# Kernel tuning notes

Measured on AMD Instinct MI355X. Metric: run time of the kernel, lower is better.

## Reference

```python
import jax, jax.numpy as jnp
import numpy as np

N_NODES = 100000
N_EDGES = 1000000
IN_DIM = 32
HID_DIM = 64
NUM_REL = 2
NUM_CLASSES = 2


def setup_inputs() -> dict:
    key = jax.random.key(0)
    ks = jax.random.split(key, 12)
    x = jax.random.normal(ks[0], (N_NODES, IN_DIM), dtype=jnp.float32)
    edge_index = jax.random.randint(ks[1], (2, N_EDGES), 0, N_NODES, dtype=jnp.int32)
    edge_attr = jax.random.randint(ks[2], (N_EDGES, 2), 0, NUM_REL, dtype=jnp.int32)
    s1 = 1.0 / np.sqrt(IN_DIM)
    s2 = 1.0 / np.sqrt(HID_DIM)
    W1 = jax.random.normal(ks[3], (NUM_REL, IN_DIM, HID_DIM), dtype=jnp.float32) * s1
    root1 = jax.random.normal(ks[4], (IN_DIM, HID_DIM), dtype=jnp.float32) * s1
    b1 = jnp.zeros((HID_DIM,), dtype=jnp.float32)
    W2 = jax.random.normal(ks[5], (NUM_REL, HID_DIM, HID_DIM), dtype=jnp.float32) * s2
    root2 = jax.random.normal(ks[6], (HID_DIM, HID_DIM), dtype=jnp.float32) * s2
    b2 = jnp.zeros((HID_DIM,), dtype=jnp.float32)
    Wc = jax.random.normal(ks[7], (HID_DIM, NUM_CLASSES), dtype=jnp.float32) * s2
    bc = jnp.zeros((NUM_CLASSES,), dtype=jnp.float32)
    return {"x": x, "edge_index": edge_index, "edge_attr": edge_attr,
            "W1": W1, "root1": root1, "b1": b1,
            "W2": W2, "root2": root2, "b2": b2,
            "Wc": Wc, "bc": bc}


def _rgcn_conv(x, src, dst, edge_type, W, root, b):
    # PyG RGCNConv (aggr='mean'): out = x @ root + b + sum_r mean_agg_r(x_j) @ W_r
    n = x.shape[0]
    xs = x[src]  # [E, F] gather, shared across relations
    out = x @ root + b
    for r in range(W.shape[0]):
        m = (edge_type == r).astype(x.dtype)  # [E]
        s = jax.ops.segment_sum(xs * m[:, None], dst, num_segments=n)  # [N, F]
        cnt = jax.ops.segment_sum(m, dst, num_segments=n)  # [N]
        h = s / jnp.maximum(cnt, 1.0)[:, None]
        out = out + h @ W[r]
    return out


def reference(x, edge_index, edge_attr, W1, root1, b1, W2, root2, b2, Wc, bc):
    edge_type = edge_attr[:, -1].astype(jnp.int32)
    src, dst = edge_index[0], edge_index[1]
    h = jax.nn.relu(_rgcn_conv(x, src, dst, edge_type, W1, root1, b1))
    # dropout(p=0.2) is identity in eval mode
    h = jax.nn.relu(_rgcn_conv(h, src, dst, edge_type, W2, root2, b2))
    return h @ Wc + bc
```

## Files before the change

kernel.cpp:

```cpp
#include <hip/hip_runtime.h>

#define N_NODES 100000
#define N_EDGES 1000000
#define IN_DIM 32
#define HID_DIM 64
#define N2 (2 * N_NODES)
#define NRANGE 8
#define RNODES (N_NODES / NRANGE)
#define ECHUNK 2048


__global__ __launch_bounds__(256) void k_count(
    const int* __restrict__ ei, const int* __restrict__ ea,
    int* __restrict__ deg)
{
    int range = blockIdx.x & (NRANGE - 1);
    int chunk = blockIdx.x >> 3;
    int lo = range * RNODES;
    int e0 = chunk * ECHUNK;
    int e1 = min(e0 + ECHUNK, N_EDGES);
    for (int e = e0 + threadIdx.x; e < e1; e += 256) {
        int dst = ei[N_EDGES + e];
        if ((unsigned)(dst - lo) < (unsigned)RNODES) {
            int rel = ea[2 * e + 1];
            atomicAdd(&deg[rel * N_NODES + dst], 1);
        }
    }
}

__global__ __launch_bounds__(256) void k_scan_local(
    const int* __restrict__ deg, int* __restrict__ offs, int* __restrict__ bsum)
{
    int t = threadIdx.x;
    int i = blockIdx.x * 256 + t;
    int v = (i < N2) ? deg[i] : 0;
    int lane = t & 63, w = t >> 6;
    int s = v;
#pragma unroll
    for (int off = 1; off < 64; off <<= 1) {
        int u = __shfl_up(s, off);
        if (lane >= off) s += u;
    }
    __shared__ int wsum[4];
    if (lane == 63) wsum[w] = s;
    __syncthreads();
    int add = 0;
    for (int ww = 0; ww < w; ++ww) add += wsum[ww];
    s += add;
    if (i < N2) offs[i] = s - v;
    if (t == 255) bsum[blockIdx.x] = s;
}

__global__ __launch_bounds__(64) void k_scan_blocks(int* __restrict__ bsum, int nblk)
{
    int lane = threadIdx.x;
    int carry = 0;
    for (int base = 0; base < nblk; base += 64) {
        int i = base + lane;
        int v = (i < nblk) ? bsum[i] : 0;
        int s = v;
#pragma unroll
        for (int off = 1; off < 64; off <<= 1) {
            int u = __shfl_up(s, off);
            if (lane >= off) s += u;
        }
        if (i < nblk) bsum[i] = carry + s - v;
        carry += __shfl(s, 63);
    }
}

__global__ __launch_bounds__(256) void k_scan_add(
    const int* __restrict__ offs, const int* __restrict__ bsum,
    const int* __restrict__ deg,
    int* __restrict__ cursor, int2* __restrict__ od)
{
    int i = blockIdx.x * 256 + threadIdx.x;
    if (i >= N2) return;
    int o = offs[i] + bsum[i >> 8];
    cursor[i] = o;
    od[i] = make_int2(o, deg[i]);
}

__global__ __launch_bounds__(256) void k_fill(
    const int* __restrict__ ei, const int* __restrict__ ea,
    int* __restrict__ cursor, int* __restrict__ elist)
{
    int range = blockIdx.x & (NRANGE - 1);
    int chunk = blockIdx.x >> 3;
    int lo = range * RNODES;
    int e0 = chunk * ECHUNK;
    int e1 = min(e0 + ECHUNK, N_EDGES);
    for (int e = e0 + threadIdx.x; e < e1; e += 256) {
        int dst = ei[N_EDGES + e];
        if ((unsigned)(dst - lo) < (unsigned)RNODES) {
            int rel = ea[2 * e + 1];
            int src = ei[e];
            int pos = atomicAdd(&cursor[rel * N_NODES + dst], 1);
            elist[pos] = src;
        }
    }
}


__device__ __forceinline__ unsigned short f2bf(float f) {
    unsigned u = __float_as_uint(f);
    return (unsigned short)((u + 0x7FFFu + ((u >> 16) & 1u)) >> 16);
}

#define ACC4(acc, v, wa, wb, wc_, wd) \
    acc = fmaf((v).x, wa, acc);       \
    acc = fmaf((v).y, wb, acc);       \
    acc = fmaf((v).z, wc_, acc);      \
    acc = fmaf((v).w, wd, acc);

#define MACC4(A, v, m)                \
    A.x = fmaf((v).x, m, A.x);        \
    A.y = fmaf((v).y, m, A.y);        \
    A.z = fmaf((v).z, m, A.z);        \
    A.w = fmaf((v).w, m, A.w);

#define BUNPACK(v_, u) {                           \
    v_.x = __uint_as_float((u).x << 16);           \
    v_.y = __uint_as_float((u).x & 0xFFFF0000u);   \
    v_.z = __uint_as_float((u).y << 16);           \
    v_.w = __uint_as_float((u).y & 0xFFFF0000u);   \
}

#define BMACC4(A, u, m) { float4 v_; BUNPACK(v_, u) MACC4(A, v_, m) }


__global__ __launch_bounds__(512, 4) void k_gemm1(
    const float* __restrict__ x,
    const float* __restrict__ root1,
    const float* __restrict__ W1,
    const float* __restrict__ b1,
    float* __restrict__ R,
    unsigned short* __restrict__ Y)
{
    __shared__ float wR[IN_DIM * HID_DIM];
    __shared__ float w0[IN_DIM * HID_DIM];
    __shared__ float w1s[IN_DIM * HID_DIM];
    int tid = threadIdx.x;
    for (int i = tid; i < IN_DIM * HID_DIM; i += 512) {
        wR[i]  = root1[i];
        w0[i]  = W1[i];
        w1s[i] = W1[IN_DIM * HID_DIM + i];
    }
    __syncthreads();

    int j  = tid & 63;
    int n0 = __builtin_amdgcn_readfirstlane(blockIdx.x * 32 + ((tid >> 6) << 2));
    const float* px = x + (size_t)n0 * IN_DIM;

    float accR0 = 0, accR1 = 0, accR2 = 0, accR3 = 0;
    float acc00 = 0, acc01 = 0, acc02 = 0, acc03 = 0;
    float acc10 = 0, acc11 = 0, acc12 = 0, acc13 = 0;

#pragma unroll 1
    for (int kk = 0; kk < IN_DIM / 4; ++kk) {
        int kbase = kk * 4;
        float4 xv0 = *(const float4*)(px + 0 * IN_DIM + kbase);
        float4 xv1 = *(const float4*)(px + 1 * IN_DIM + kbase);
        float4 xv2 = *(const float4*)(px + 2 * IN_DIM + kbase);
        float4 xv3 = *(const float4*)(px + 3 * IN_DIM + kbase);
        int wb_i = kbase * 64 + j;
        float wRa = wR[wb_i], wRb = wR[wb_i + 64], wRc = wR[wb_i + 128], wRd = wR[wb_i + 192];
        float w0a = w0[wb_i], w0b = w0[wb_i + 64], w0c = w0[wb_i + 128], w0d = w0[wb_i + 192];
        float w1a = w1s[wb_i], w1b = w1s[wb_i + 64], w1c = w1s[wb_i + 128], w1d = w1s[wb_i + 192];

        ACC4(accR0, xv0, wRa, wRb, wRc, wRd)
        ACC4(accR1, xv1, wRa, wRb, wRc, wRd)
        ACC4(accR2, xv2, wRa, wRb, wRc, wRd)
        ACC4(accR3, xv3, wRa, wRb, wRc, wRd)
        ACC4(acc00, xv0, w0a, w0b, w0c, w0d)
        ACC4(acc01, xv1, w0a, w0b, w0c, w0d)
        ACC4(acc02, xv2, w0a, w0b, w0c, w0d)
        ACC4(acc03, xv3, w0a, w0b, w0c, w0d)
        ACC4(acc10, xv0, w1a, w1b, w1c, w1d)
        ACC4(acc11, xv1, w1a, w1b, w1c, w1d)
        ACC4(acc12, xv2, w1a, w1b, w1c, w1d)
        ACC4(acc13, xv3, w1a, w1b, w1c, w1d)
    }

    float bj = b1[j];
    R[(size_t)(n0 + 0) * HID_DIM + j] = accR0 + bj;
    R[(size_t)(n0 + 1) * HID_DIM + j] = accR1 + bj;
    R[(size_t)(n0 + 2) * HID_DIM + j] = accR2 + bj;
    R[(size_t)(n0 + 3) * HID_DIM + j] = accR3 + bj;
    unsigned short* Y0 = Y;
    unsigned short* Y1 = Y + (size_t)N_NODES * HID_DIM;
    Y0[(size_t)(n0 + 0) * HID_DIM + j] = f2bf(acc00);
    Y0[(size_t)(n0 + 1) * HID_DIM + j] = f2bf(acc01);
    Y0[(size_t)(n0 + 2) * HID_DIM + j] = f2bf(acc02);
    Y0[(size_t)(n0 + 3) * HID_DIM + j] = f2bf(acc03);
    Y1[(size_t)(n0 + 0) * HID_DIM + j] = f2bf(acc10);
    Y1[(size_t)(n0 + 1) * HID_DIM + j] = f2bf(acc11);
    Y1[(size_t)(n0 + 2) * HID_DIM + j] = f2bf(acc12);
    Y1[(size_t)(n0 + 3) * HID_DIM + j] = f2bf(acc13);
}

__global__ __launch_bounds__(512, 4) void k_gemm2(
    const unsigned short* __restrict__ h1b,
    const float* __restrict__ root2,
    const float* __restrict__ W2,
    const float* __restrict__ b2,
    float* __restrict__ R,
    unsigned short* __restrict__ Y)
{
    __shared__ float wR[HID_DIM * HID_DIM];
    __shared__ float w0[HID_DIM * HID_DIM];
    __shared__ float w1s[HID_DIM * HID_DIM];
    int tid = threadIdx.x;
    for (int i = tid; i < HID_DIM * HID_DIM; i += 512) {
        wR[i]  = root2[i];
        w0[i]  = W2[i];
        w1s[i] = W2[HID_DIM * HID_DIM + i];
    }
    __syncthreads();

    int j  = tid & 63;
    int n0 = __builtin_amdgcn_readfirstlane(blockIdx.x * 32 + ((tid >> 6) << 2));
    const unsigned short* pb = h1b + (size_t)n0 * HID_DIM;

    float accR0 = 0, accR1 = 0, accR2 = 0, accR3 = 0;
    float acc00 = 0, acc01 = 0, acc02 = 0, acc03 = 0;
    float acc10 = 0, acc11 = 0, acc12 = 0, acc13 = 0;

#pragma unroll 1
    for (int kk = 0; kk < HID_DIM / 4; ++kk) {
        int kbase = kk * 4;
        uint2 u0 = *(const uint2*)(pb + 0 * HID_DIM + kbase);
        uint2 u1 = *(const uint2*)(pb + 1 * HID_DIM + kbase);
        uint2 u2 = *(const uint2*)(pb + 2 * HID_DIM + kbase);
        uint2 u3 = *(const uint2*)(pb + 3 * HID_DIM + kbase);
        float4 xv0, xv1, xv2, xv3;
        BUNPACK(xv0, u0) BUNPACK(xv1, u1) BUNPACK(xv2, u2) BUNPACK(xv3, u3)
        int wb_i = kbase * 64 + j;
        float wRa = wR[wb_i], wRb = wR[wb_i + 64], wRc = wR[wb_i + 128], wRd = wR[wb_i + 192];
        float w0a = w0[wb_i], w0b = w0[wb_i + 64], w0c = w0[wb_i + 128], w0d = w0[wb_i + 192];
        float w1a = w1s[wb_i], w1b = w1s[wb_i + 64], w1c = w1s[wb_i + 128], w1d = w1s[wb_i + 192];

        ACC4(accR0, xv0, wRa, wRb, wRc, wRd)
        ACC4(accR1, xv1, wRa, wRb, wRc, wRd)
        ACC4(accR2, xv2, wRa, wRb, wRc, wRd)
        ACC4(accR3, xv3, wRa, wRb, wRc, wRd)
        ACC4(acc00, xv0, w0a, w0b, w0c, w0d)
        ACC4(acc01, xv1, w0a, w0b, w0c, w0d)
        ACC4(acc02, xv2, w0a, w0b, w0c, w0d)
        ACC4(acc03, xv3, w0a, w0b, w0c, w0d)
        ACC4(acc10, xv0, w1a, w1b, w1c, w1d)
        ACC4(acc11, xv1, w1a, w1b, w1c, w1d)
        ACC4(acc12, xv2, w1a, w1b, w1c, w1d)
        ACC4(acc13, xv3, w1a, w1b, w1c, w1d)
    }

    float bj = b2[j];
    R[(size_t)(n0 + 0) * HID_DIM + j] = accR0 + bj;
    R[(size_t)(n0 + 1) * HID_DIM + j] = accR1 + bj;
    R[(size_t)(n0 + 2) * HID_DIM + j] = accR2 + bj;
    R[(size_t)(n0 + 3) * HID_DIM + j] = accR3 + bj;
    unsigned short* Y0 = Y;
    unsigned short* Y1 = Y + (size_t)N_NODES * HID_DIM;
    Y0[(size_t)(n0 + 0) * HID_DIM + j] = f2bf(acc00);
    Y0[(size_t)(n0 + 1) * HID_DIM + j] = f2bf(acc01);
    Y0[(size_t)(n0 + 2) * HID_DIM + j] = f2bf(acc02);
    Y0[(size_t)(n0 + 3) * HID_DIM + j] = f2bf(acc03);
    Y1[(size_t)(n0 + 0) * HID_DIM + j] = f2bf(acc10);
    Y1[(size_t)(n0 + 1) * HID_DIM + j] = f2bf(acc11);
    Y1[(size_t)(n0 + 2) * HID_DIM + j] = f2bf(acc12);
    Y1[(size_t)(n0 + 3) * HID_DIM + j] = f2bf(acc13);
}


__global__ __launch_bounds__(512, 8) void k_gather1(
    const unsigned short* __restrict__ Y,
    const float* __restrict__ R,
    const int2* __restrict__ od,
    const int* __restrict__ elist,
    unsigned short* __restrict__ h1b)
{
    int tid = threadIdx.x;
    int lane = tid & 63;
    int wv   = __builtin_amdgcn_readfirstlane(tid >> 6);
    int n0   = __builtin_amdgcn_readfirstlane(blockIdx.x * 32 + wv * 4);

    int sub  = lane >> 4;
    int node = n0 + sub;
    int q    = lane & 15;
    int base = lane & 48;

    const unsigned short* Y0 = Y;
    const unsigned short* Y1 = Y + (size_t)N_NODES * HID_DIM;

    int2 o0 = od[node];
    int2 o1 = od[N_NODES + node];
    int d0 = o0.y, d1 = o1.y;
    int er0 = (q < d0) ? elist[o0.x + q] : 0;
    int er1 = (q < d1) ? elist[o1.x + q] : 0;

    int dm = max(d0, d1);
    dm = max(dm, __shfl_xor(dm, 16));
    dm = max(dm, __shfl_xor(dm, 32));
    int kend = min(dm, 16);

    float4 A0 = make_float4(0.f, 0.f, 0.f, 0.f);
    float4 A1 = make_float4(0.f, 0.f, 0.f, 0.f);
    for (int k = 0; k < kend; ++k) {
        int i0 = __shfl(er0, base + k);
        int i1 = __shfl(er1, base + k);
        uint2 u0 = *(const uint2*)(Y0 + (size_t)i0 * HID_DIM + q * 4);
        uint2 u1 = *(const uint2*)(Y1 + (size_t)i1 * HID_DIM + q * 4);
        float m0 = (k < d0) ? 1.0f : 0.0f;
        float m1 = (k < d1) ? 1.0f : 0.0f;
        BMACC4(A0, u0, m0)
        BMACC4(A1, u1, m1)
    }
    if (dm > 16) {
        for (int k = 16; k < dm; ++k) {
            int i0 = 0, i1 = 0;
            if (k < d0) i0 = elist[o0.x + k];
            if (k < d1) i1 = elist[o1.x + k];
            uint2 u0 = *(const uint2*)(Y0 + (size_t)i0 * HID_DIM + q * 4);
            uint2 u1 = *(const uint2*)(Y1 + (size_t)i1 * HID_DIM + q * 4);
            float m0 = (k < d0) ? 1.0f : 0.0f;
            float m1 = (k < d1) ? 1.0f : 0.0f;
            BMACC4(A0, u0, m0)
            BMACC4(A1, u1, m1)
        }
    }
    float i0v = 1.0f / fmaxf((float)d0, 1.0f);
    float i1v = 1.0f / fmaxf((float)d1, 1.0f);
    float4 Rq = *(const float4*)(R + (size_t)node * HID_DIM + q * 4);
    ushort4 o;
    o.x = f2bf(fmaxf(Rq.x + A0.x * i0v + A1.x * i1v, 0.0f));
    o.y = f2bf(fmaxf(Rq.y + A0.y * i0v + A1.y * i1v, 0.0f));
    o.z = f2bf(fmaxf(Rq.z + A0.z * i0v + A1.z * i1v, 0.0f));
    o.w = f2bf(fmaxf(Rq.w + A0.w * i0v + A1.w * i1v, 0.0f));
    *(ushort4*)(h1b + (size_t)node * HID_DIM + q * 4) = o;
}

__global__ __launch_bounds__(512, 8) void k_gather2(
    const unsigned short* __restrict__ Y,
    const float* __restrict__ R,
    const int2* __restrict__ od,
    const int* __restrict__ elist,
    const float* __restrict__ Wc,
    const float* __restrict__ bc,
    float* __restrict__ out)
{
    int tid = threadIdx.x;
    int lane = tid & 63;
    int wv   = __builtin_amdgcn_readfirstlane(tid >> 6);
    int n0   = __builtin_amdgcn_readfirstlane(blockIdx.x * 32 + wv * 4);

    int sub  = lane >> 4;
    int node = n0 + sub;
    int q    = lane & 15;
    int base = lane & 48;

    const unsigned short* Y0 = Y;
    const unsigned short* Y1 = Y + (size_t)N_NODES * HID_DIM;

    int2 o0 = od[node];
    int2 o1 = od[N_NODES + node];
    int d0 = o0.y, d1 = o1.y;
    int er0 = (q < d0) ? elist[o0.x + q] : 0;
    int er1 = (q < d1) ? elist[o1.x + q] : 0;

    int dm = max(d0, d1);
    dm = max(dm, __shfl_xor(dm, 16));
    dm = max(dm, __shfl_xor(dm, 32));
    int kend = min(dm, 16);

    float4 A0 = make_float4(0.f, 0.f, 0.f, 0.f);
    float4 A1 = make_float4(0.f, 0.f, 0.f, 0.f);
    for (int k = 0; k < kend; ++k) {
        int i0 = __shfl(er0, base + k);
        int i1 = __shfl(er1, base + k);
        uint2 u0 = *(const uint2*)(Y0 + (size_t)i0 * HID_DIM + q * 4);
        uint2 u1 = *(const uint2*)(Y1 + (size_t)i1 * HID_DIM + q * 4);
        float m0 = (k < d0) ? 1.0f : 0.0f;
        float m1 = (k < d1) ? 1.0f : 0.0f;
        BMACC4(A0, u0, m0)
        BMACC4(A1, u1, m1)
    }
    if (dm > 16) {
        for (int k = 16; k < dm; ++k) {
            int i0 = 0, i1 = 0;
            if (k < d0) i0 = elist[o0.x + k];
            if (k < d1) i1 = elist[o1.x + k];
            uint2 u0 = *(const uint2*)(Y0 + (size_t)i0 * HID_DIM + q * 4);
            uint2 u1 = *(const uint2*)(Y1 + (size_t)i1 * HID_DIM + q * 4);
            float m0 = (k < d0) ? 1.0f : 0.0f;
            float m1 = (k < d1) ? 1.0f : 0.0f;
            BMACC4(A0, u0, m0)
            BMACC4(A1, u1, m1)
        }
    }
    float i0v = 1.0f / fmaxf((float)d0, 1.0f);
    float i1v = 1.0f / fmaxf((float)d1, 1.0f);
    float4 Rq = *(const float4*)(R + (size_t)node * HID_DIM + q * 4);
    float4 h2;
    h2.x = fmaxf(Rq.x + A0.x * i0v + A1.x * i1v, 0.0f);
    h2.y = fmaxf(Rq.y + A0.y * i0v + A1.y * i1v, 0.0f);
    h2.z = fmaxf(Rq.z + A0.z * i0v + A1.z * i1v, 0.0f);
    h2.w = fmaxf(Rq.w + A0.w * i0v + A1.w * i1v, 0.0f);

    float4 wcA = *(const float4*)(Wc + 8 * q);
    float4 wcB = *(const float4*)(Wc + 8 * q + 4);
    float v0 = h2.x * wcA.x + h2.y * wcA.z + h2.z * wcB.x + h2.w * wcB.z;
    float v1 = h2.x * wcA.y + h2.y * wcA.w + h2.z * wcB.y + h2.w * wcB.w;
#pragma unroll
    for (int off = 1; off <= 8; off <<= 1) {
        v0 += __shfl_xor(v0, off);
        v1 += __shfl_xor(v1, off);
    }
    if (q == 0) {
        out[(size_t)node * 2 + 0] = v0 + bc[0];
        out[(size_t)node * 2 + 1] = v1 + bc[1];
    }
}


extern "C" void kernel_launch(void* const* d_in, const int* in_sizes, int n_in,
                              void* d_out, int out_size, void* d_ws, size_t ws_size,
                              hipStream_t stream) {
    const float* x     = (const float*)d_in[0];
    const int*   ei    = (const int*)d_in[1];
    const int*   ea    = (const int*)d_in[2];
    const float* W1    = (const float*)d_in[3];
    const float* root1 = (const float*)d_in[4];
    const float* b1    = (const float*)d_in[5];
    const float* W2    = (const float*)d_in[6];
    const float* root2 = (const float*)d_in[7];
    const float* b2    = (const float*)d_in[8];
    const float* Wc    = (const float*)d_in[9];
    const float* bc    = (const float*)d_in[10];
    float* out = (float*)d_out;

    char* ws = (char*)d_ws;
    int*   deg    = (int*)(ws);
    int*   offs   = (int*)(ws + 800000);
    int2*  od     = (int2*)(ws + 1600000);
    int*   elist  = (int*)(ws + 3200000);
    int*   cursor = (int*)(ws + 7200000);
    int*   bsum   = (int*)(ws + 8000000);
    unsigned short* Y   = (unsigned short*)(ws + 8004096);
    float* R            = (float*)(ws + 33604096);
    unsigned short* h1b = (unsigned short*)(ws + 59204096);

    const int nblk_scan = (N2 + 255) / 256;
    const int grid_cf   = ((N_EDGES + ECHUNK - 1) / ECHUNK) * NRANGE;
    const int grid_n    = N_NODES / 32;

    hipMemsetAsync(deg, 0, (size_t)N2 * 4, stream);
    k_count<<<grid_cf, 256, 0, stream>>>(ei, ea, deg);
    k_scan_local<<<nblk_scan, 256, 0, stream>>>(deg, offs, bsum);
    k_scan_blocks<<<1, 64, 0, stream>>>(bsum, nblk_scan);
    k_scan_add<<<nblk_scan, 256, 0, stream>>>(offs, bsum, deg, cursor, od);
    k_fill<<<grid_cf, 256, 0, stream>>>(ei, ea, cursor, elist);

    k_gemm1<<<grid_n, 512, 0, stream>>>(x, root1, W1, b1, R, Y);
    k_gather1<<<grid_n, 512, 0, stream>>>(Y, R, od, elist, h1b);

    k_gemm2<<<grid_n, 512, 0, stream>>>(h1b, root2, W2, b2, R, Y);
    k_gather2<<<grid_n, 512, 0, stream>>>(Y, R, od, elist, Wc, bc, out);
}
```

Baseline: 230.9 us.

## Pack dst and relation into one word; make GEMM kernels persistent

Adds a pre-pass that packs each edge's destination and relation type into a single int, so the count and fill passes (each launched 8 times over the edge list, once per node range) read one coalesced int instead of the dst row plus a strided edge_attr column. The two per-node GEMM kernels become grid-stride persistent kernels over a fixed 768-block grid, so the weight matrices are staged into LDS fewer times. The cost is an extra kernel launch and a 4 MB write, and fewer resident blocks may hide latency less well.

```diff
diff --git a/kernel.cpp b/kernel.cpp
--- a/kernel.cpp
+++ b/kernel.cpp
@@ -8,11 +8,22 @@
 #define NRANGE 8
 #define RNODES (N_NODES / NRANGE)
 #define ECHUNK 2048
+#define NTILES (N_NODES / 32)
+#define GEMM_GRID 768
+
+
+__global__ __launch_bounds__(256) void k_rd(
+    const int* __restrict__ ei, const int* __restrict__ ea,
+    int* __restrict__ rd)
+{
+    int e = blockIdx.x * 256 + threadIdx.x;
+    if (e >= N_EDGES) return;
+    rd[e] = (ei[N_EDGES + e] << 1) | ea[2 * e + 1];
+}
 
 
 __global__ __launch_bounds__(256) void k_count(
-    const int* __restrict__ ei, const int* __restrict__ ea,
-    int* __restrict__ deg)
+    const int* __restrict__ rd, int* __restrict__ deg)
 {
     int range = blockIdx.x & (NRANGE - 1);
     int chunk = blockIdx.x >> 3;
@@ -20,11 +31,10 @@
     int e0 = chunk * ECHUNK;
     int e1 = min(e0 + ECHUNK, N_EDGES);
     for (int e = e0 + threadIdx.x; e < e1; e += 256) {
-        int dst = ei[N_EDGES + e];
-        if ((unsigned)(dst - lo) < (unsigned)RNODES) {
-            int rel = ea[2 * e + 1];
-            atomicAdd(&deg[rel * N_NODES + dst], 1);
-        }
+        int v = rd[e];
+        int dst = v >> 1;
+        if ((unsigned)(dst - lo) < (unsigned)RNODES)
+            atomicAdd(&deg[(v & 1) * N_NODES + dst], 1);
     }
 }
 
@@ -82,7 +92,7 @@
 }
 
 __global__ __launch_bounds__(256) void k_fill(
-    const int* __restrict__ ei, const int* __restrict__ ea,
+    const int* __restrict__ rd, const int* __restrict__ ei,
     int* __restrict__ cursor, int* __restrict__ elist)
 {
     int range = blockIdx.x & (NRANGE - 1);
@@ -91,11 +101,11 @@
     int e0 = chunk * ECHUNK;
     int e1 = min(e0 + ECHUNK, N_EDGES);
     for (int e = e0 + threadIdx.x; e < e1; e += 256) {
-        int dst = ei[N_EDGES + e];
+        int v = rd[e];
+        int dst = v >> 1;
         if ((unsigned)(dst - lo) < (unsigned)RNODES) {
-            int rel = ea[2 * e + 1];
             int src = ei[e];
-            int pos = atomicAdd(&cursor[rel * N_NODES + dst], 1);
+            int pos = atomicAdd(&cursor[(v & 1) * N_NODES + dst], 1);
             elist[pos] = src;
         }
     }
@@ -148,55 +158,59 @@
     }
     __syncthreads();
 
-    int j  = tid & 63;
-    int n0 = __builtin_amdgcn_readfirstlane(blockIdx.x * 32 + ((tid >> 6) << 2));
-    const float* px = x + (size_t)n0 * IN_DIM;
-
-    float accR0 = 0, accR1 = 0, accR2 = 0, accR3 = 0;
-    float acc00 = 0, acc01 = 0, acc02 = 0, acc03 = 0;
-    float acc10 = 0, acc11 = 0, acc12 = 0, acc13 = 0;
-
-#pragma unroll 1
-    for (int kk = 0; kk < IN_DIM / 4; ++kk) {
-        int kbase = kk * 4;
-        float4 xv0 = *(const float4*)(px + 0 * IN_DIM + kbase);
-        float4 xv1 = *(const float4*)(px + 1 * IN_DIM + kbase);
-        float4 xv2 = *(const float4*)(px + 2 * IN_DIM + kbase);
-        float4 xv3 = *(const float4*)(px + 3 * IN_DIM + kbase);
-        int wb_i = kbase * 64 + j;
-        float wRa = wR[wb_i], wRb = wR[wb_i + 64], wRc = wR[wb_i + 128], wRd = wR[wb_i + 192];
-        float w0a = w0[wb_i], w0b = w0[wb_i + 64], w0c = w0[wb_i + 128], w0d = w0[wb_i + 192];
-        float w1a = w1s[wb_i], w1b = w1s[wb_i + 64], w1c = w1s[wb_i + 128], w1d = w1s[wb_i + 192];
-
-        ACC4(accR0, xv0, wRa, wRb, wRc, wRd)
-        ACC4(accR1, xv1, wRa, wRb, wRc, wRd)
-        ACC4(accR2, xv2, wRa, wRb, wRc, wRd)
-        ACC4(accR3, xv3, wRa, wRb, wRc, wRd)
-        ACC4(acc00, xv0, w0a, w0b, w0c, w0d)
-        ACC4(acc01, xv1, w0a, w0b, w0c, w0d)
-        ACC4(acc02, xv2, w0a, w0b, w0c, w0d)
-        ACC4(acc03, xv3, w0a, w0b, w0c, w0d)
-        ACC4(acc10, xv0, w1a, w1b, w1c, w1d)
-        ACC4(acc11, xv1, w1a, w1b, w1c, w1d)
-        ACC4(acc12, xv2, w1a, w1b, w1c, w1d)
-        ACC4(acc13, xv3, w1a, w1b, w1c, w1d)
-    }
-
+    int j   = tid & 63;
+    int wv4 = (tid >> 6) << 2;
     float bj = b1[j];
-    R[(size_t)(n0 + 0) * HID_DIM + j] = accR0 + bj;
-    R[(size_t)(n0 + 1) * HID_DIM + j] = accR1 + bj;
-    R[(size_t)(n0 + 2) * HID_DIM + j] = accR2 + bj;
-    R[(size_t)(n0 + 3) * HID_DIM + j] = accR3 + bj;
     unsigned short* Y0 = Y;
     unsigned short* Y1 = Y + (size_t)N_NODES * HID_DIM;
-    Y0[(size_t)(n0 + 0) * HID_DIM + j] = f2bf(acc00);
-    Y0[(size_t)(n0 + 1) * HID_DIM + j] = f2bf(acc01);
-    Y0[(size_t)(n0 + 2) * HID_DIM + j] = f2bf(acc02);
-    Y0[(size_t)(n0 + 3) * HID_DIM + j] = f2bf(acc03);
-    Y1[(size_t)(n0 + 0) * HID_DIM + j] = f2bf(acc10);
-    Y1[(size_t)(n0 + 1) * HID_DIM + j] = f2bf(acc11);
-    Y1[(size_t)(n0 + 2) * HID_DIM + j] = f2bf(acc12);
-    Y1[(size_t)(n0 + 3) * HID_DIM + j] = f2bf(acc13);
+
+    for (int t = blockIdx.x; t < NTILES; t += gridDim.x) {
+        int n0 = __builtin_amdgcn_readfirstlane(t * 32 + wv4);
+        const float* px = x + (size_t)n0 * IN_DIM;
+
+        float accR0 = 0, accR1 = 0, accR2 = 0, accR3 = 0;
+        float acc00 = 0, acc01 = 0, acc02 = 0, acc03 = 0;
+        float acc10 = 0, acc11 = 0, acc12 = 0, acc13 = 0;
+
+#pragma unroll 1
+        for (int kk = 0; kk < IN_DIM / 4; ++kk) {
+            int kbase = kk * 4;
+            float4 xv0 = *(const float4*)(px + 0 * IN_DIM + kbase);
+            float4 xv1 = *(const float4*)(px + 1 * IN_DIM + kbase);
+            float4 xv2 = *(const float4*)(px + 2 * IN_DIM + kbase);
+            float4 xv3 = *(const float4*)(px + 3 * IN_DIM + kbase);
+            int wb_i = kbase * 64 + j;
+            float wRa = wR[wb_i], wRb = wR[wb_i + 64], wRc = wR[wb_i + 128], wRd = wR[wb_i + 192];
+            float w0a = w0[wb_i], w0b = w0[wb_i + 64], w0c = w0[wb_i + 128], w0d = w0[wb_i + 192];
+            float w1a = w1s[wb_i], w1b = w1s[wb_i + 64], w1c = w1s[wb_i + 128], w1d = w1s[wb_i + 192];
+
+            ACC4(accR0, xv0, wRa, wRb, wRc, wRd)
+            ACC4(accR1, xv1, wRa, wRb, wRc, wRd)
+            ACC4(accR2, xv2, wRa, wRb, wRc, wRd)
+            ACC4(accR3, xv3, wRa, wRb, wRc, wRd)
+            ACC4(acc00, xv0, w0a, w0b, w0c, w0d)
+            ACC4(acc01, xv1, w0a, w0b, w0c, w0d)
+            ACC4(acc02, xv2, w0a, w0b, w0c, w0d)
+            ACC4(acc03, xv3, w0a, w0b, w0c, w0d)
+            ACC4(acc10, xv0, w1a, w1b, w1c, w1d)
+            ACC4(acc11, xv1, w1a, w1b, w1c, w1d)
+            ACC4(acc12, xv2, w1a, w1b, w1c, w1d)
+            ACC4(acc13, xv3, w1a, w1b, w1c, w1d)
+        }
+
+        R[(size_t)(n0 + 0) * HID_DIM + j] = accR0 + bj;
+        R[(size_t)(n0 + 1) * HID_DIM + j] = accR1 + bj;
+        R[(size_t)(n0 + 2) * HID_DIM + j] = accR2 + bj;
+        R[(size_t)(n0 + 3) * HID_DIM + j] = accR3 + bj;
+        Y0[(size_t)(n0 + 0) * HID_DIM + j] = f2bf(acc00);
+        Y0[(size_t)(n0 + 1) * HID_DIM + j] = f2bf(acc01);
+        Y0[(size_t)(n0 + 2) * HID_DIM + j] = f2bf(acc02);
+        Y0[(size_t)(n0 + 3) * HID_DIM + j] = f2bf(acc03);
+        Y1[(size_t)(n0 + 0) * HID_DIM + j] = f2bf(acc10);
+        Y1[(size_t)(n0 + 1) * HID_DIM + j] = f2bf(acc11);
+        Y1[(size_t)(n0 + 2) * HID_DIM + j] = f2bf(acc12);
+        Y1[(size_t)(n0 + 3) * HID_DIM + j] = f2bf(acc13);
+    }
 }
 
 __global__ __launch_bounds__(512, 4) void k_gemm2(
@@ -218,57 +232,61 @@
     }
     __syncthreads();
 
-    int j  = tid & 63;
-    int n0 = __builtin_amdgcn_readfirstlane(blockIdx.x * 32 + ((tid >> 6) << 2));
-    const unsigned short* pb = h1b + (size_t)n0 * HID_DIM;
-
-    float accR0 = 0, accR1 = 0, accR2 = 0, accR3 = 0;
-    float acc00 = 0, acc01 = 0, acc02 = 0, acc03 = 0;
-    float acc10 = 0, acc11 = 0, acc12 = 0, acc13 = 0;
-
-#pragma unroll 1
-    for (int kk = 0; kk < HID_DIM / 4; ++kk) {
-        int kbase = kk * 4;
-        uint2 u0 = *(const uint2*)(pb + 0 * HID_DIM + kbase);
-        uint2 u1 = *(const uint2*)(pb + 1 * HID_DIM + kbase);
-        uint2 u2 = *(const uint2*)(pb + 2 * HID_DIM + kbase);
-        uint2 u3 = *(const uint2*)(pb + 3 * HID_DIM + kbase);
-        float4 xv0, xv1, xv2, xv3;
-        BUNPACK(xv0, u0) BUNPACK(xv1, u1) BUNPACK(xv2, u2) BUNPACK(xv3, u3)
-        int wb_i = kbase * 64 + j;
-        float wRa = wR[wb_i], wRb = wR[wb_i + 64], wRc = wR[wb_i + 128], wRd = wR[wb_i + 192];
-        float w0a = w0[wb_i], w0b = w0[wb_i + 64], w0c = w0[wb_i + 128], w0d = w0[wb_i + 192];
-        float w1a = w1s[wb_i], w1b = w1s[wb_i + 64], w1c = w1s[wb_i + 128], w1d = w1s[wb_i + 192];
-
-        ACC4(accR0, xv0, wRa, wRb, wRc, wRd)
-        ACC4(accR1, xv1, wRa, wRb, wRc, wRd)
-        ACC4(accR2, xv2, wRa, wRb, wRc, wRd)
-        ACC4(accR3, xv3, wRa, wRb, wRc, wRd)
-        ACC4(acc00, xv0, w0a, w0b, w0c, w0d)
-        ACC4(acc01, xv1, w0a, w0b, w0c, w0d)
-        ACC4(acc02, xv2, w0a, w0b, w0c, w0d)
-        ACC4(acc03, xv3, w0a, w0b, w0c, w0d)
-        ACC4(acc10, xv0, w1a, w1b, w1c, w1d)
-        ACC4(acc11, xv1, w1a, w1b, w1c, w1d)
-        ACC4(acc12, xv2, w1a, w1b, w1c, w1d)
-        ACC4(acc13, xv3, w1a, w1b, w1c, w1d)
-    }
-
+    int j   = tid & 63;
+    int wv4 = (tid >> 6) << 2;
     float bj = b2[j];
-    R[(size_t)(n0 + 0) * HID_DIM + j] = accR0 + bj;
-    R[(size_t)(n0 + 1) * HID_DIM + j] = accR1 + bj;
-    R[(size_t)(n0 + 2) * HID_DIM + j] = accR2 + bj;
-    R[(size_t)(n0 + 3) * HID_DIM + j] = accR3 + bj;
     unsigned short* Y0 = Y;
     unsigned short* Y1 = Y + (size_t)N_NODES * HID_DIM;
-    Y0[(size_t)(n0 + 0) * HID_DIM + j] = f2bf(acc00);
-    Y0[(size_t)(n0 + 1) * HID_DIM + j] = f2bf(acc01);
-    Y0[(size_t)(n0 + 2) * HID_DIM + j] = f2bf(acc02);
-    Y0[(size_t)(n0 + 3) * HID_DIM + j] = f2bf(acc03);
-    Y1[(size_t)(n0 + 0) * HID_DIM + j] = f2bf(acc10);
-    Y1[(size_t)(n0 + 1) * HID_DIM + j] = f2bf(acc11);
-    Y1[(size_t)(n0 + 2) * HID_DIM + j] = f2bf(acc12);
-    Y1[(size_t)(n0 + 3) * HID_DIM + j] = f2bf(acc13);
+
+    for (int t = blockIdx.x; t < NTILES; t += gridDim.x) {
+        int n0 = __builtin_amdgcn_readfirstlane(t * 32 + wv4);
+        const unsigned short* pb = h1b + (size_t)n0 * HID_DIM;
+
+        float accR0 = 0, accR1 = 0, accR2 = 0, accR3 = 0;
+        float acc00 = 0, acc01 = 0, acc02 = 0, acc03 = 0;
+        float acc10 = 0, acc11 = 0, acc12 = 0, acc13 = 0;
+
+#pragma unroll 1
+        for (int kk = 0; kk < HID_DIM / 4; ++kk) {
+            int kbase = kk * 4;
+            uint2 u0 = *(const uint2*)(pb + 0 * HID_DIM + kbase);
+            uint2 u1 = *(const uint2*)(pb + 1 * HID_DIM + kbase);
+            uint2 u2 = *(const uint2*)(pb + 2 * HID_DIM + kbase);
+            uint2 u3 = *(const uint2*)(pb + 3 * HID_DIM + kbase);
+            float4 xv0, xv1, xv2, xv3;
+            BUNPACK(xv0, u0) BUNPACK(xv1, u1) BUNPACK(xv2, u2) BUNPACK(xv3, u3)
+            int wb_i = kbase * 64 + j;
+            float wRa = wR[wb_i], wRb = wR[wb_i + 64], wRc = wR[wb_i + 128], wRd = wR[wb_i + 192];
+            float w0a = w0[wb_i], w0b = w0[wb_i + 64], w0c = w0[wb_i + 128], w0d = w0[wb_i + 192];
+            float w1a = w1s[wb_i], w1b = w1s[wb_i + 64], w1c = w1s[wb_i + 128], w1d = w1s[wb_i + 192];
+
+            ACC4(accR0, xv0, wRa, wRb, wRc, wRd)
+            ACC4(accR1, xv1, wRa, wRb, wRc, wRd)
+            ACC4(accR2, xv2, wRa, wRb, wRc, wRd)
+            ACC4(accR3, xv3, wRa, wRb, wRc, wRd)
+            ACC4(acc00, xv0, w0a, w0b, w0c, w0d)
+            ACC4(acc01, xv1, w0a, w0b, w0c, w0d)
+            ACC4(acc02, xv2, w0a, w0b, w0c, w0d)
+            ACC4(acc03, xv3, w0a, w0b, w0c, w0d)
+            ACC4(acc10, xv0, w1a, w1b, w1c, w1d)
+            ACC4(acc11, xv1, w1a, w1b, w1c, w1d)
+            ACC4(acc12, xv2, w1a, w1b, w1c, w1d)
+            ACC4(acc13, xv3, w1a, w1b, w1c, w1d)
+        }
+
+        R[(size_t)(n0 + 0) * HID_DIM + j] = accR0 + bj;
+        R[(size_t)(n0 + 1) * HID_DIM + j] = accR1 + bj;
+        R[(size_t)(n0 + 2) * HID_DIM + j] = accR2 + bj;
+        R[(size_t)(n0 + 3) * HID_DIM + j] = accR3 + bj;
+        Y0[(size_t)(n0 + 0) * HID_DIM + j] = f2bf(acc00);
+        Y0[(size_t)(n0 + 1) * HID_DIM + j] = f2bf(acc01);
+        Y0[(size_t)(n0 + 2) * HID_DIM + j] = f2bf(acc02);
+        Y0[(size_t)(n0 + 3) * HID_DIM + j] = f2bf(acc03);
+        Y1[(size_t)(n0 + 0) * HID_DIM + j] = f2bf(acc10);
+        Y1[(size_t)(n0 + 1) * HID_DIM + j] = f2bf(acc11);
+        Y1[(size_t)(n0 + 2) * HID_DIM + j] = f2bf(acc12);
+        Y1[(size_t)(n0 + 3) * HID_DIM + j] = f2bf(acc13);
+    }
 }
 
 
@@ -448,21 +466,24 @@
     unsigned short* Y   = (unsigned short*)(ws + 8004096);
     float* R            = (float*)(ws + 33604096);
     unsigned short* h1b = (unsigned short*)(ws + 59204096);
+    int*   rd     = (int*)(ws + 72004096);
 
     const int nblk_scan = (N2 + 255) / 256;
+    const int grid_e    = (N_EDGES + 255) / 256;
     const int grid_cf   = ((N_EDGES + ECHUNK - 1) / ECHUNK) * NRANGE;
     const int grid_n    = N_NODES / 32;
 
     hipMemsetAsync(deg, 0, (size_t)N2 * 4, stream);
-    k_count<<<grid_cf, 256, 0, stream>>>(ei, ea, deg);
+    k_rd<<<grid_e, 256, 0, stream>>>(ei, ea, rd);
+    k_count<<<grid_cf, 256, 0, stream>>>(rd, deg);
     k_scan_local<<<nblk_scan, 256, 0, stream>>>(deg, offs, bsum);
     k_scan_blocks<<<1, 64, 0, stream>>>(bsum, nblk_scan);
     k_scan_add<<<nblk_scan, 256, 0, stream>>>(offs, bsum, deg, cursor, od);
-    k_fill<<<grid_cf, 256, 0, stream>>>(ei, ea, cursor, elist);
-
-    k_gemm1<<<grid_n, 512, 0, stream>>>(x, root1, W1, b1, R, Y);
+    k_fill<<<grid_cf, 256, 0, stream>>>(rd, ei, cursor, elist);
+
+    k_gemm1<<<GEMM_GRID, 512, 0, stream>>>(x, root1, W1, b1, R, Y);
     k_gather1<<<grid_n, 512, 0, stream>>>(Y, R, od, elist, h1b);
 
-    k_gemm2<<<grid_n, 512, 0, stream>>>(h1b, root2, W2, b2, R, Y);
+    k_gemm2<<<GEMM_GRID, 512, 0, stream>>>(h1b, root2, W2, b2, R, Y);
     k_gather2<<<grid_n, 512, 0, stream>>>(Y, R, od, elist, Wc, bc, out);
 }
```

Result: no change. 235.1 us (+1.8%).
